# Kernel tuning notes

Hardware: AMD Instinct MI355X
Metric: run time of the kernel (lower is better)

The kernel has to match this reference:

```python
import jax, jax.numpy as jnp
import numpy as np

EPS = 1e-6

def _ln(x, g, b):
    mu = jnp.mean(x, axis=-1, keepdims=True)
    var = jnp.mean(jnp.square(x - mu), axis=-1, keepdims=True)
    return (x - mu) * jax.lax.rsqrt(var + EPS) * g + b

def setup_inputs() -> dict:
    key = jax.random.key(0)
    ks = jax.random.split(key, 8)
    B, T, D = 4, 4096, 1024
    H = 16
    Dff = 4 * D
    s = 1.0 / np.sqrt(D)
    sf = 1.0 / np.sqrt(Dff)
    return {
        "x": jax.random.normal(ks[0], (B, T, D), dtype=jnp.float32),
        "wq": jax.random.uniform(ks[1], (D, D), jnp.float32, -s, s),
        "wk": jax.random.uniform(ks[2], (D, D), jnp.float32, -s, s),
        "wv": jax.random.uniform(ks[3], (D, D), jnp.float32, -s, s),
        "wo": jax.random.uniform(ks[4], (D, D), jnp.float32, -s, s),
        "ln1_g": jnp.ones((D,), jnp.float32),
        "ln1_b": jnp.zeros((D,), jnp.float32),
        "w1": jax.random.uniform(ks[5], (D, Dff), jnp.float32, -s, s),
        "b1": jnp.zeros((Dff,), jnp.float32),
        "w2": jax.random.uniform(ks[6], (Dff, D), jnp.float32, -sf, sf),
        "b2": jnp.zeros((D,), jnp.float32),
        "ln2_g": jnp.ones((D,), jnp.float32),
        "ln2_b": jnp.zeros((D,), jnp.float32),
    }

def reference(x, wq, wk, wv, wo, ln1_g, ln1_b, w1, b1, w2, b2, ln2_g, ln2_b):
    B, T, D = x.shape
    H = 16
    dk = D // H
    x1 = _ln(x, ln1_g, ln1_b)
    q = (x1 @ wq).reshape(B, T, H, dk)
    k = (x1 @ wk).reshape(B, T, H, dk)
    v = (x1 @ wv).reshape(B, T, H, dk)
    # NOTE: faithful to source -- attention mixes HEADS at each token position
    # attn[b,t,h,g] = softmax_g( sum_d q[b,t,h,d]*k[b,t,g,d] / sqrt(dk) )
    attn = jax.nn.softmax(jnp.einsum('bthd,btgd->bthg', q / np.sqrt(dk), k), axis=-1)
    o = jnp.einsum('bthg,btgd->bthd', attn, v)
    # faithful head-major reshape: transpose(1,2).contiguous().view(B,T,-1)
    o = jnp.transpose(o, (0, 2, 1, 3)).reshape(B, T, H * dk)
    o = o @ wo
    q2 = _ln(o + x, ln1_g, ln1_b)  # same layer_norm params reused
    h = jax.nn.gelu(q2 @ w1 + b1, approximate=False)
    y = h @ w2 + b2 + q2
    return _ln(y, ln2_g, ln2_b)
```

## Files before the change

### kernel.cpp

```cpp
#include <hip/hip_runtime.h>


typedef __attribute__((ext_vector_type(8))) short s16x8;
typedef __attribute__((ext_vector_type(4))) short s16x4;
typedef __attribute__((ext_vector_type(16))) float f32x16;

__device__ __forceinline__ short f2bf(float x) {
  unsigned u = __builtin_bit_cast(unsigned, x);
  u = (u + 0x7FFFu + ((u >> 16) & 1u)) >> 16;
  return (short)u;
}
__device__ __forceinline__ float bf2f(short s) {
  unsigned u = ((unsigned)(unsigned short)s) << 16;
  return __builtin_bit_cast(float, u);
}

__device__ __forceinline__ void ld_g2l16(const short* g, short* l) {
  __builtin_amdgcn_global_load_lds(
      (const __attribute__((address_space(1))) void*)g,
      (__attribute__((address_space(3))) void*)l, 16, 0, 0);
}

__device__ __forceinline__ float fast_gelu(float v) {
  float y = 0.7978845608f * (v + 0.044715f * v * v * v);
  float ay = fabsf(y);
  float t = __expf(-2.0f * ay);
  float th = (1.0f - t) * __frcp_rn(1.0f + t);
  th = (y >= 0.f) ? th : -th;
  return 0.5f * v * (1.0f + th);
}

template <int EPI>
__global__ __launch_bounds__(256, 2) void gemm_bt(
    const short* __restrict__ A, const short* __restrict__ BT,
    void* __restrict__ outp, const float* __restrict__ bias, int M, int N,
    int K) {
  __shared__ __align__(16) short As[2][256 * 32];
  __shared__ __align__(16) short Bs[2][128 * 32];

  const int lane = threadIdx.x & 63;
  const int wave = threadIdx.x >> 6;
  const int bm = blockIdx.x, bn = blockIdx.y;
  const int m31 = lane & 31;
  const int h = lane >> 5;
  const int wm = (wave >> 1) * 128;
  const int wn = (wave & 1) * 64;

  f32x16 acc[4][2];
#pragma unroll
  for (int i = 0; i < 4; i++)
#pragma unroll
    for (int j = 0; j < 2; j++)
#pragma unroll
      for (int r = 0; r < 16; r++) acc[i][j][r] = 0.f;

  const int srow = lane >> 2;
  const int sch = (lane & 3) ^ (srow & 3);
  const short* gA = A + (size_t)(bm * 256) * K + sch * 8;
  const short* gB = BT + (size_t)(bn * 128) * K + sch * 8;

  const int xkey = (m31 & 3);

  for (int k0 = 0; k0 < K; k0 += 64) {
#pragma unroll
    for (int p = 0; p < 2; p++) {
      const int kk = k0 + p * 32;
#pragma unroll
      for (int c = 0; c < 4; c++) {
        const int s = wave * 4 + c;
        ld_g2l16(gA + (size_t)(s * 16 + srow) * K + kk, As[p] + s * 512);
      }
#pragma unroll
      for (int c = 0; c < 2; c++) {
        const int s = wave * 2 + c;
        ld_g2l16(gB + (size_t)(s * 16 + srow) * K + kk, Bs[p] + s * 512);
      }
    }
    __syncthreads();

#pragma unroll
    for (int p = 0; p < 2; p++) {
#pragma unroll
      for (int ks = 0; ks < 2; ks++) {
        const int g = ks * 2 + h;
        const int co = (g ^ xkey) * 8;
        s16x8 a8[4], b8[2];
#pragma unroll
        for (int i = 0; i < 4; i++)
          a8[i] = *(const s16x8*)(As[p] + (wm + i * 32 + m31) * 32 + co);
#pragma unroll
        for (int j = 0; j < 2; j++)
          b8[j] = *(const s16x8*)(Bs[p] + (wn + j * 32 + m31) * 32 + co);
#pragma unroll
        for (int i = 0; i < 4; i++)
#pragma unroll
          for (int j = 0; j < 2; j++)
            acc[i][j] = __builtin_amdgcn_mfma_f32_32x32x16_bf16(
                a8[i], b8[j], acc[i][j], 0, 0, 0);
      }
    }
    __syncthreads();
  }

  const int mb = bm * 256 + wm, nb = bn * 128 + wn;
#pragma unroll
  for (int i = 0; i < 4; i++) {
#pragma unroll
    for (int j = 0; j < 2; j++) {
#pragma unroll
      for (int r = 0; r < 16; r++) {
        const size_t row = (size_t)(mb + i * 32 + (r & 3) + 8 * (r >> 2) + 4 * h);
        const int col = nb + j * 32 + m31;
        float v = acc[i][j][r];
        if constexpr (EPI == 0) {
          ((short*)outp)[row * N + col] = f2bf(v);
        } else if constexpr (EPI == 1) {
          ((float*)outp)[row * N + col] = v;
        } else if constexpr (EPI == 2) {
          v += bias[col];
          ((short*)outp)[row * N + col] = f2bf(fast_gelu(v));
        } else {
          float prev = ((float*)outp)[row * N + col];
          v += prev;
          if (bias) v += bias[col];
          ((float*)outp)[row * N + col] = v;
        }
      }
    }
  }
}

__global__ __launch_bounds__(256) void ln_k(
    const float* __restrict__ in, const float* __restrict__ add,
    const float* __restrict__ g, const float* __restrict__ b,
    float* __restrict__ outf, short* __restrict__ outb) {
  const int row = blockIdx.x;
  const size_t off = (size_t)row * 1024;
  const int t = threadIdx.x;
  float4 v = ((const float4*)(in + off))[t];
  if (add) {
    float4 w = ((const float4*)(add + off))[t];
    v.x += w.x; v.y += w.y; v.z += w.z; v.w += w.w;
  }
  float s = v.x + v.y + v.z + v.w;
  float ss = v.x * v.x + v.y * v.y + v.z * v.z + v.w * v.w;
#pragma unroll
  for (int o = 32; o > 0; o >>= 1) {
    s += __shfl_xor(s, o, 64);
    ss += __shfl_xor(ss, o, 64);
  }
  __shared__ float ps[4], pss[4];
  const int lane = t & 63, wave = t >> 6;
  if (lane == 0) { ps[wave] = s; pss[wave] = ss; }
  __syncthreads();
  s = ps[0] + ps[1] + ps[2] + ps[3];
  ss = pss[0] + pss[1] + pss[2] + pss[3];
  const float mean = s * (1.0f / 1024.0f);
  const float var = ss * (1.0f / 1024.0f) - mean * mean;
  const float rstd = rsqrtf(var + 1e-6f);
  const float4 gv = ((const float4*)g)[t];
  const float4 bv = ((const float4*)b)[t];
  float4 o4;
  o4.x = (v.x - mean) * rstd * gv.x + bv.x;
  o4.y = (v.y - mean) * rstd * gv.y + bv.y;
  o4.z = (v.z - mean) * rstd * gv.z + bv.z;
  o4.w = (v.w - mean) * rstd * gv.w + bv.w;
  if (outf) ((float4*)(outf + off))[t] = o4;
  if (outb) {
    s16x4 ob;
    ob[0] = f2bf(o4.x); ob[1] = f2bf(o4.y);
    ob[2] = f2bf(o4.z); ob[3] = f2bf(o4.w);
    *(s16x4*)(outb + off + t * 4) = ob;
  }
}

__global__ __launch_bounds__(256) void wconv_t(const float* __restrict__ W,
                                               short* __restrict__ WT, int K,
                                               int N) {
  __shared__ float tile[32][33];
  const int t = threadIdx.x;
  const int c = t & 31, r = t >> 5;
  const int n0 = blockIdx.x * 32, k0 = blockIdx.y * 32;
#pragma unroll
  for (int rr = r; rr < 32; rr += 8)
    tile[rr][c] = W[(size_t)(k0 + rr) * N + n0 + c];
  __syncthreads();
#pragma unroll
  for (int rr = r; rr < 32; rr += 8)
    WT[(size_t)(n0 + rr) * K + k0 + c] = f2bf(tile[c][rr]);
}

__global__ __launch_bounds__(256) void attn_k(const short* __restrict__ qkv,
                                              short* __restrict__ omix) {
  __shared__ float Qs[4][16][64];
  __shared__ float Ks[4][16][64];
  __shared__ float Vs[4][16][64];
  __shared__ float Ps[4][16][16];
  const int lane = threadIdx.x & 63;
  const int wave = threadIdx.x >> 6;
  const int tok = blockIdx.x * 4 + wave;
  const short* base = qkv + (size_t)tok * 3072;

#pragma unroll
  for (int half = 0; half < 2; half++) {
    const int e = half * 512 + lane * 8;
    const int h = e >> 6, d = e & 63;
    s16x8 rq = *(const s16x8*)(base + e);
    s16x8 rk = *(const s16x8*)(base + 1024 + e);
    s16x8 rv = *(const s16x8*)(base + 2048 + e);
#pragma unroll
    for (int j = 0; j < 8; j++) {
      Qs[wave][h][d + j] = bf2f(rq[j]);
      Ks[wave][h][d + j] = bf2f(rk[j]);
      Vs[wave][h][d + j] = bf2f(rv[j]);
    }
  }
  __syncthreads();

  const int h = lane & 15;
  const int g0 = (lane >> 4) * 4;
  float sc[4] = {0.f, 0.f, 0.f, 0.f};
  for (int d = 0; d < 64; d++) {
    const float qv = Qs[wave][h][d];
#pragma unroll
    for (int i = 0; i < 4; i++) sc[i] += qv * Ks[wave][g0 + i][d];
  }
#pragma unroll
  for (int i = 0; i < 4; i++) sc[i] *= 0.125f;
  float m = fmaxf(fmaxf(sc[0], sc[1]), fmaxf(sc[2], sc[3]));
  m = fmaxf(m, __shfl_xor(m, 16, 64));
  m = fmaxf(m, __shfl_xor(m, 32, 64));
  float e[4], sum = 0.f;
#pragma unroll
  for (int i = 0; i < 4; i++) { e[i] = __expf(sc[i] - m); sum += e[i]; }
  sum += __shfl_xor(sum, 16, 64);
  sum += __shfl_xor(sum, 32, 64);
  const float inv = __frcp_rn(sum);
#pragma unroll
  for (int i = 0; i < 4; i++) Ps[wave][h][g0 + i] = e[i] * inv;
  __syncthreads();

  const int d0 = (lane >> 4) * 16;
  float o[16];
#pragma unroll
  for (int dd = 0; dd < 16; dd++) o[dd] = 0.f;
  for (int gg = 0; gg < 16; gg++) {
    const float pv = Ps[wave][h][gg];
#pragma unroll
    for (int dd = 0; dd < 16; dd++) o[dd] += pv * Vs[wave][gg][d0 + dd];
  }

  const int b = tok >> 12, t = tok & 4095;
  const size_t dst =
      ((size_t)(b * 4096 + h * 256 + (t >> 4))) * 1024 + (t & 15) * 64 + d0;
  s16x8 w0, w1;
#pragma unroll
  for (int j = 0; j < 8; j++) { w0[j] = f2bf(o[j]); w1[j] = f2bf(o[8 + j]); }
  *(s16x8*)(omix + dst) = w0;
  *(s16x8*)(omix + dst + 8) = w1;
}

extern "C" void kernel_launch(void* const* d_in, const int* in_sizes, int n_in,
                              void* d_out, int out_size, void* d_ws,
                              size_t ws_size, hipStream_t stream) {
  const float* x    = (const float*)d_in[0];
  const float* wq   = (const float*)d_in[1];
  const float* wk   = (const float*)d_in[2];
  const float* wv   = (const float*)d_in[3];
  const float* wo   = (const float*)d_in[4];
  const float* ln1g = (const float*)d_in[5];
  const float* ln1b = (const float*)d_in[6];
  const float* w1   = (const float*)d_in[7];
  const float* b1   = (const float*)d_in[8];
  const float* w2   = (const float*)d_in[9];
  const float* b2   = (const float*)d_in[10];
  const float* ln2g = (const float*)d_in[11];
  const float* ln2b = (const float*)d_in[12];
  float* out = (float*)d_out;

  char* ws = (char*)d_ws;
  const size_t MB = 1024ull * 1024ull;
  const size_t NEEDED = 152 * MB;
  if (ws_size < NEEDED) return;

  short* QKV  = (short*)(ws + 0);
  short* Q2B  = (short*)(ws + 0);
  short* Hbuf = (short*)(ws + 32 * MB);
  short* X1 = (short*)(ws + 96 * MB);
  short* WQKVT = (short*)(ws + 128 * MB);
  short* WOT   = (short*)(ws + 134 * MB);
  short* W1T   = (short*)(ws + 136 * MB);
  short* W2aT  = (short*)(ws + 144 * MB);
  short* W2bT  = (short*)(ws + 148 * MB);

  const dim3 B256(256);

  wconv_t<<<dim3(32, 32), B256, 0, stream>>>(wq, WQKVT, 1024, 1024);
  wconv_t<<<dim3(32, 32), B256, 0, stream>>>(wk, WQKVT + 1024 * 1024, 1024, 1024);
  wconv_t<<<dim3(32, 32), B256, 0, stream>>>(wv, WQKVT + 2048 * 1024, 1024, 1024);
  wconv_t<<<dim3(32, 32), B256, 0, stream>>>(wo, WOT, 1024, 1024);
  wconv_t<<<dim3(128, 32), B256, 0, stream>>>(w1, W1T, 1024, 4096);
  wconv_t<<<dim3(32, 64), B256, 0, stream>>>(w2, W2aT, 2048, 1024);
  wconv_t<<<dim3(32, 64), B256, 0, stream>>>(w2 + 2048 * 1024, W2bT, 2048, 1024);

  ln_k<<<16384, B256, 0, stream>>>(x, nullptr, ln1g, ln1b, nullptr, X1);

  gemm_bt<0><<<dim3(64, 24), B256, 0, stream>>>(X1, WQKVT, QKV, nullptr,
                                                16384, 3072, 1024);

  attn_k<<<4096, B256, 0, stream>>>(QKV, X1);

  gemm_bt<1><<<dim3(64, 8), B256, 0, stream>>>(X1, WOT, out, nullptr, 16384,
                                               1024, 1024);

  ln_k<<<16384, B256, 0, stream>>>(out, x, ln1g, ln1b, out, Q2B);

  gemm_bt<2><<<dim3(64, 16), B256, 0, stream>>>(Q2B, W1T, Hbuf, b1, 16384,
                                                2048, 1024);
  gemm_bt<4><<<dim3(64, 8), B256, 0, stream>>>(Hbuf, W2aT, out, nullptr,
                                               16384, 1024, 2048);

  gemm_bt<2><<<dim3(64, 16), B256, 0, stream>>>(Q2B, W1T + 2048 * 1024, Hbuf,
                                                b1 + 2048, 16384, 2048, 1024);
  gemm_bt<4><<<dim3(64, 8), B256, 0, stream>>>(Hbuf, W2bT, out, b2, 16384,
                                               1024, 2048);

  ln_k<<<16384, B256, 0, stream>>>(out, nullptr, ln2g, ln2b, out, nullptr);
}
```

Before: 927.7 us.

## Double-buffer GEMM K-loop with prefetch and change the LDS swizzle key

The bf16 MFMA GEMM main loop no longer loads two 32-wide K slices and then computes on both behind two barriers. It now prefetches the next 32-wide slice into the alternate LDS buffer while computing on the current one, with a single barrier per iteration. This is meant to overlap global-to-LDS transfer with MFMA work and cut barrier stalls. The XOR swizzle key also changes from row&3 to (row>>2)&3 on both the write and read sides, which alters the LDS bank-conflict pattern. The risk is that correctness now depends on the asynchronous LDS loads being complete at the barrier, and the swizzle change may raise or lower bank conflicts.

Result: no change. 938.6 us (+1.2%).

```diff
diff --git a/kernel.cpp b/kernel.cpp
--- a/kernel.cpp
+++ b/kernel.cpp
@@ -55,51 +55,62 @@
       for (int r = 0; r < 16; r++) acc[i][j][r] = 0.f;
 
   const int srow = lane >> 2;
-  const int sch = (lane & 3) ^ (srow & 3);
+  const int sch = (lane & 3) ^ ((lane >> 4) & 3);
   const short* gA = A + (size_t)(bm * 256) * K + sch * 8;
   const short* gB = BT + (size_t)(bn * 128) * K + sch * 8;
 
-  const int xkey = (m31 & 3);
-
-  for (int k0 = 0; k0 < K; k0 += 64) {
-#pragma unroll
-    for (int p = 0; p < 2; p++) {
-      const int kk = k0 + p * 32;
+  const int xkey = (m31 >> 2) & 3;
+
+  const int iters = K >> 5;
+
+#pragma unroll
+  for (int c = 0; c < 4; c++) {
+    const int s = wave * 4 + c;
+    ld_g2l16(gA + (size_t)(s * 16 + srow) * K, As[0] + s * 512);
+  }
+#pragma unroll
+  for (int c = 0; c < 2; c++) {
+    const int s = wave * 2 + c;
+    ld_g2l16(gB + (size_t)(s * 16 + srow) * K, Bs[0] + s * 512);
+  }
+
+  for (int n = 0; n < iters; n++) {
+    __syncthreads();
+
+    if (n + 1 < iters) {
+      const int kk = (n + 1) << 5;
+      const int nb2 = (n + 1) & 1;
 #pragma unroll
       for (int c = 0; c < 4; c++) {
         const int s = wave * 4 + c;
-        ld_g2l16(gA + (size_t)(s * 16 + srow) * K + kk, As[p] + s * 512);
+        ld_g2l16(gA + (size_t)(s * 16 + srow) * K + kk, As[nb2] + s * 512);
       }
 #pragma unroll
       for (int c = 0; c < 2; c++) {
         const int s = wave * 2 + c;
-        ld_g2l16(gB + (size_t)(s * 16 + srow) * K + kk, Bs[p] + s * 512);
+        ld_g2l16(gB + (size_t)(s * 16 + srow) * K + kk, Bs[nb2] + s * 512);
       }
     }
-    __syncthreads();
-
-#pragma unroll
-    for (int p = 0; p < 2; p++) {
-#pragma unroll
-      for (int ks = 0; ks < 2; ks++) {
-        const int g = ks * 2 + h;
-        const int co = (g ^ xkey) * 8;
-        s16x8 a8[4], b8[2];
-#pragma unroll
-        for (int i = 0; i < 4; i++)
-          a8[i] = *(const s16x8*)(As[p] + (wm + i * 32 + m31) * 32 + co);
+
+    const int cb = n & 1;
+#pragma unroll
+    for (int ks = 0; ks < 2; ks++) {
+      const int g = ks * 2 + h;
+      const int co = (g ^ xkey) * 8;
+      s16x8 a8[4], b8[2];
+#pragma unroll
+      for (int i = 0; i < 4; i++)
+        a8[i] = *(const s16x8*)(As[cb] + (wm + i * 32 + m31) * 32 + co);
+#pragma unroll
+      for (int j = 0; j < 2; j++)
+        b8[j] = *(const s16x8*)(Bs[cb] + (wn + j * 32 + m31) * 32 + co);
+#pragma unroll
+      for (int i = 0; i < 4; i++)
 #pragma unroll
         for (int j = 0; j < 2; j++)
-          b8[j] = *(const s16x8*)(Bs[p] + (wn + j * 32 + m31) * 32 + co);
-#pragma unroll
-        for (int i = 0; i < 4; i++)
-#pragma unroll
-          for (int j = 0; j < 2; j++)
-            acc[i][j] = __builtin_amdgcn_mfma_f32_32x32x16_bf16(
-                a8[i], b8[j], acc[i][j], 0, 0, 0);
-      }
+          acc[i][j] = __builtin_amdgcn_mfma_f32_32x32x16_bf16(
+              a8[i], b8[j], acc[i][j], 0, 0, 0);
     }
-    __syncthreads();
   }
 
   const int mb = bm * 256 + wm, nb = bn * 128 + wn;
@@ -109,7 +120,8 @@
     for (int j = 0; j < 2; j++) {
 #pragma unroll
       for (int r = 0; r < 16; r++) {
-        const size_t row = (size_t)(mb + i * 32 + (r & 3) + 8 * (r >> 2) + 4 * h);
+        const size_t row =
+            (size_t)(mb + i * 32 + (r & 3) + 8 * (r >> 2) + 4 * h);
         const int col = nb + j * 32 + m31;
         float v = acc[i][j][r];
         if constexpr (EPI == 0) {
```
